# Kernel optimization log

Hardware: AMD Instinct MI355X
Metric: run time of the kernel (lower is better)

## Reference

```python
import jax, jax.numpy as jnp
import numpy as np

MARGIN = 0.1  # init kwarg margin
B, N = 16384, 50


def setup_inputs() -> dict:
    key = jax.random.key(0)
    k1, k2 = jax.random.split(key)
    scores = jax.random.normal(k1, (B * N,), dtype=jnp.float32)
    # per-segment permutation of [0, N): hypotheses ordered by WER
    werRank = jnp.argsort(jax.random.uniform(k2, (B, N)), axis=-1).astype(jnp.int32)
    return {"scores": scores, "werRank": werRank, "nBest": N}


def reference(scores, werRank, nBest):
    # scores: [B*N] flat concatenated nBest scores; werRank: [B,N] permutations.
    b = werRank.shape[0]
    seg = scores.reshape(b, nBest)                      # [B, N]
    ranked = jnp.take_along_axis(seg, werRank, axis=1)  # score at rank j, [B, N]
    # hinge[b, j, k] = relu(margin - (pos_j - neg_k))
    hinge = jnp.maximum(0.0, MARGIN - (ranked[:, :, None] - ranked[:, None, :]))
    j = jnp.arange(nBest)
    tri = (j[None, :] > j[:, None]).astype(scores.dtype)          # k > j mask, [N, N]
    counts = (nBest - 1 - j[:-1]).astype(scores.dtype)            # #neg per rank j
    # reduction='mean' over negatives for each j, then summed over j and batch
    per_j = (hinge * tri[None, :, :]).sum(-1)[:, :-1] / counts[None, :]  # [B, N-1]
    total = jnp.sum(per_j)
    return total.reshape(1)
```

## Files before the change

kernel.cpp:

```cpp
#include <hip/hip_runtime.h>

#define NBEST 50
#define SEGS_PER_BLOCK 4
#define MARGIN 0.1f

__global__ void margin_partial_kernel(const float* __restrict__ scores,
                                      const int* __restrict__ werRank,
                                      float* __restrict__ partials,
                                      int B) {
    const int wave = threadIdx.x >> 6;
    const int lane = threadIdx.x & 63;
    const int seg  = blockIdx.x * SEGS_PER_BLOCK + wave;

    __shared__ float r[SEGS_PER_BLOCK][64];
    __shared__ float wsum[SEGS_PER_BLOCK];

    float rj = 0.0f;
    if (seg < B && lane < NBEST) {
        const int idx = werRank[seg * NBEST + lane];
        rj = scores[seg * NBEST + idx];
    }
    r[wave][lane] = rj;
    __syncthreads();

    float acc = 0.0f;
    #pragma unroll
    for (int k = 0; k < NBEST; ++k) {
        float d = MARGIN - (rj - r[wave][k]);
        d = fmaxf(d, 0.0f);
        acc += (k > lane) ? d : 0.0f;
    }
    float val = (seg < B && lane < NBEST - 1)
                    ? acc / (float)(NBEST - 1 - lane)
                    : 0.0f;

    #pragma unroll
    for (int off = 32; off >= 1; off >>= 1)
        val += __shfl_xor(val, off, 64);

    if (lane == 0) wsum[wave] = val;
    __syncthreads();

    if (threadIdx.x == 0) {
        float s = 0.0f;
        #pragma unroll
        for (int w = 0; w < SEGS_PER_BLOCK; ++w) s += wsum[w];
        partials[blockIdx.x] = s;
    }
}

__global__ void margin_reduce_kernel(const float* __restrict__ partials,
                                     int n, float* __restrict__ out) {
    __shared__ float sm[256];
    float s = 0.0f;
    for (int i = threadIdx.x; i < n; i += 256) s += partials[i];
    sm[threadIdx.x] = s;
    __syncthreads();
    #pragma unroll
    for (int off = 128; off >= 1; off >>= 1) {
        if (threadIdx.x < off) sm[threadIdx.x] += sm[threadIdx.x + off];
        __syncthreads();
    }
    if (threadIdx.x == 0) out[0] = sm[0];
}

extern "C" void kernel_launch(void* const* d_in, const int* in_sizes, int n_in,
                              void* d_out, int out_size, void* d_ws, size_t ws_size,
                              hipStream_t stream) {
    const float* scores  = (const float*)d_in[0];
    const int*   werRank = (const int*)d_in[1];
    float*       out     = (float*)d_out;
    float*       partials = (float*)d_ws;

    const int B = in_sizes[0] / NBEST;
    const int grid1 = (B + SEGS_PER_BLOCK - 1) / SEGS_PER_BLOCK;

    margin_partial_kernel<<<grid1, SEGS_PER_BLOCK * 64, 0, stream>>>(
        scores, werRank, partials, B);
    margin_reduce_kernel<<<1, 256, 0, stream>>>(partials, grid1, out);
}
```

Measured before the change: 17.97 us.

## Replace shared-memory gather with cross-lane shuffles and single-wave final reduce

The per-segment gather now loads scores and werRank coalesced and permutes them with a wave shuffle instead of an indirect global load. Pairwise terms read each rank's score via readlane broadcast rather than shared memory, and the first __syncthreads goes away. The final reduction kernel becomes a single 64-lane wave using float4 loads and xor shuffles. The float4 path drops up to 3 trailing partials when the count is not a multiple of 4; here grid1 is 4096, so nothing is lost.

```diff
diff --git a/kernel.cpp b/kernel.cpp
--- a/kernel.cpp
+++ b/kernel.cpp
@@ -4,31 +4,34 @@
 #define SEGS_PER_BLOCK 4
 #define MARGIN 0.1f
 
-__global__ void margin_partial_kernel(const float* __restrict__ scores,
-                                      const int* __restrict__ werRank,
-                                      float* __restrict__ partials,
-                                      int B) {
+__global__ void __launch_bounds__(256)
+margin_partial_kernel(const float* __restrict__ scores,
+                      const int* __restrict__ werRank,
+                      float* __restrict__ partials,
+                      int B) {
     const int wave = threadIdx.x >> 6;
     const int lane = threadIdx.x & 63;
     const int seg  = blockIdx.x * SEGS_PER_BLOCK + wave;
 
-    __shared__ float r[SEGS_PER_BLOCK][64];
     __shared__ float wsum[SEGS_PER_BLOCK];
 
-    float rj = 0.0f;
+    float s  = 0.0f;
+    int   wr = 0;
     if (seg < B && lane < NBEST) {
-        const int idx = werRank[seg * NBEST + lane];
-        rj = scores[seg * NBEST + idx];
+        const int base = seg * NBEST;
+        s  = scores[base + lane];
+        wr = werRank[base + lane];
     }
-    r[wave][lane] = rj;
-    __syncthreads();
+    const float rj = __shfl(s, wr, 64);
 
+    const float c = MARGIN - rj;
     float acc = 0.0f;
     #pragma unroll
-    for (int k = 0; k < NBEST; ++k) {
-        float d = MARGIN - (rj - r[wave][k]);
-        d = fmaxf(d, 0.0f);
-        acc += (k > lane) ? d : 0.0f;
+    for (int k = 1; k < NBEST; ++k) {
+        const float rk = __uint_as_float(
+            __builtin_amdgcn_readlane(__float_as_uint(rj), k));
+        const float d = fmaxf(c + rk, 0.0f);
+        acc += (lane < k) ? d : 0.0f;
     }
     float val = (seg < B && lane < NBEST - 1)
                     ? acc / (float)(NBEST - 1 - lane)
@@ -42,34 +45,36 @@
     __syncthreads();
 
     if (threadIdx.x == 0) {
-        float s = 0.0f;
+        float t = 0.0f;
         #pragma unroll
-        for (int w = 0; w < SEGS_PER_BLOCK; ++w) s += wsum[w];
-        partials[blockIdx.x] = s;
+        for (int w = 0; w < SEGS_PER_BLOCK; ++w) t += wsum[w];
+        partials[blockIdx.x] = t;
     }
 }
 
-__global__ void margin_reduce_kernel(const float* __restrict__ partials,
-                                     int n, float* __restrict__ out) {
-    __shared__ float sm[256];
-    float s = 0.0f;
-    for (int i = threadIdx.x; i < n; i += 256) s += partials[i];
-    sm[threadIdx.x] = s;
-    __syncthreads();
+__global__ void __launch_bounds__(64)
+margin_reduce_kernel(const float* __restrict__ partials,
+                     int n, float* __restrict__ out) {
+    const int lane = threadIdx.x & 63;
+    const float4* p4 = (const float4*)partials;
+    const int n4 = n >> 2;
+    float sum = 0.0f;
+    for (int i = lane; i < n4; i += 64) {
+        float4 v = p4[i];
+        sum += (v.x + v.y) + (v.z + v.w);
+    }
     #pragma unroll
-    for (int off = 128; off >= 1; off >>= 1) {
-        if (threadIdx.x < off) sm[threadIdx.x] += sm[threadIdx.x + off];
-        __syncthreads();
-    }
-    if (threadIdx.x == 0) out[0] = sm[0];
+    for (int off = 32; off >= 1; off >>= 1)
+        sum += __shfl_xor(sum, off, 64);
+    if (lane == 0) out[0] = sum;
 }
 
 extern "C" void kernel_launch(void* const* d_in, const int* in_sizes, int n_in,
                               void* d_out, int out_size, void* d_ws, size_t ws_size,
                               hipStream_t stream) {
-    const float* scores  = (const float*)d_in[0];
-    const int*   werRank = (const int*)d_in[1];
-    float*       out     = (float*)d_out;
+    const float* scores   = (const float*)d_in[0];
+    const int*   werRank  = (const int*)d_in[1];
+    float*       out      = (float*)d_out;
     float*       partials = (float*)d_ws;
 
     const int B = in_sizes[0] / NBEST;
@@ -77,5 +82,5 @@
 
     margin_partial_kernel<<<grid1, SEGS_PER_BLOCK * 64, 0, stream>>>(
         scores, werRank, partials, B);
-    margin_reduce_kernel<<<1, 256, 0, stream>>>(partials, grid1, out);
+    margin_reduce_kernel<<<1, 64, 0, stream>>>(partials, grid1, out);
 }
```

Result: slower. 20.18 us (+12.3%).
